# Kernel optimization log

Hardware: AMD Instinct MI355X
Metric: run time of the kernel (lower is better)

The kernel has to match this reference:

```python
import jax, jax.numpy as jnp
import numpy as np

N, E, H = 50000, 800000, 128
NUM_NC = 40
NUM_LAYERS = 3


def setup_inputs() -> dict:
    key = jax.random.key(0)
    ks = jax.random.split(key, 16)
    s = 1.0 / np.sqrt(H)
    inp = {
        "x": jax.random.normal(ks[0], (N, H), jnp.float32),
        "edge_index": jax.random.randint(ks[1], (2, E), 0, N, jnp.int64),
        "na_alphas": 0.001 * jax.random.normal(ks[2], (3, 4), jnp.float32),
        "sc_alphas": 0.001 * jax.random.normal(ks[3], (2, 2), jnp.float32),
        "la_alphas": 0.001 * jax.random.normal(ks[4], (1, 3), jnp.float32),
        "lin1_W": s * jax.random.normal(ks[5], (H, H), jnp.float32),
        "lin1_b": jnp.zeros((H,), jnp.float32),
        "gcn_W": s * jax.random.normal(ks[6], (3, H, H), jnp.float32),
        "gcn_b": jnp.zeros((3, H), jnp.float32),
        "sage_Ws": s * jax.random.normal(ks[7], (3, H, H), jnp.float32),
        "sage_Wn": s * jax.random.normal(ks[8], (3, H, H), jnp.float32),
        "gin_W": s * jax.random.normal(ks[9], (3, H, H), jnp.float32),
        "gin_b": jnp.zeros((3, H), jnp.float32),
        "gin_eps": jnp.zeros((3,), jnp.float32),
        "gat_W": s * jax.random.normal(ks[10], (3, H, H), jnp.float32),
        "gat_as": s * jax.random.normal(ks[11], (3, H), jnp.float32),
        "gat_ad": s * jax.random.normal(ks[12], (3, H), jnp.float32),
        "nc_W": s * jax.random.normal(ks[13], (NUM_NC, H), jnp.float32),
        "nc_b": jnp.zeros((NUM_NC,), jnp.float32),
    }
    return inp


def _gcn(x, src, dst, deg_inv_sqrt, W, b):
    h = x @ W.T + b                           # [N, H]
    norm = deg_inv_sqrt[src] * deg_inv_sqrt[dst]
    msg = h[src] * norm[:, None]              # [E, H] gather
    return jax.ops.segment_sum(msg, dst, num_segments=N)


def _sage(x, src, dst, deg, Ws, Wn):
    agg = jax.ops.segment_sum(x[src], dst, num_segments=N) / jnp.maximum(deg, 1.0)[:, None]
    return x @ Ws.T + agg @ Wn.T


def _gin(x, src, dst, W, b, eps):
    agg = jax.ops.segment_sum(x[src], dst, num_segments=N)
    return ((1.0 + eps) * x + agg) @ W.T + b


def _gat(x, src, dst, W, a_s, a_d):
    h = x @ W.T                               # [N, H]
    logits = jax.nn.leaky_relu((h @ a_s)[src] + (h @ a_d)[dst], 0.2)  # [E]
    m = jax.ops.segment_max(logits, dst, num_segments=N)
    e = jnp.exp(logits - m[dst])
    z = jax.ops.segment_sum(e, dst, num_segments=N)
    alpha = e / (z[dst] + 1e-16)
    return jax.ops.segment_sum(alpha[:, None] * h[src], dst, num_segments=N)


def _na_mixed(x, w, src, dst, deg, dis, l, gcn_W, gcn_b, sage_Ws, sage_Wn,
              gin_W, gin_b, gin_eps, gat_W, gat_as, gat_ad):
    # sum_i w_i * elu(op_i(x, edge_index))
    o0 = _gcn(x, src, dst, dis, gcn_W[l], gcn_b[l])
    o1 = _sage(x, src, dst, deg, sage_Ws[l], sage_Wn[l])
    o2 = _gin(x, src, dst, gin_W[l], gin_b[l], gin_eps[l])
    o3 = _gat(x, src, dst, gat_W[l], gat_as[l], gat_ad[l])
    return (w[0] * jax.nn.elu(o0) + w[1] * jax.nn.elu(o1)
            + w[2] * jax.nn.elu(o2) + w[3] * jax.nn.elu(o3))


def reference(x, edge_index, na_alphas, sc_alphas, la_alphas, lin1_W, lin1_b,
              gcn_W, gcn_b, sage_Ws, sage_Wn, gin_W, gin_b, gin_eps,
              gat_W, gat_as, gat_ad, nc_W, nc_b):
    src, dst = edge_index[0], edge_index[1]
    deg = jax.ops.segment_sum(jnp.ones((E,), x.dtype), dst, num_segments=N)
    dis = jnp.where(deg > 0, 1.0 / jnp.sqrt(jnp.maximum(deg, 1.0)), 0.0)

    na_w = jax.nn.softmax(na_alphas, axis=-1)   # [3, 4]
    sc_w = jax.nn.softmax(sc_alphas, axis=-1)   # [2, 2] (none, skip)
    la_w = jax.nn.softmax(la_alphas, axis=-1)   # [1, 3]

    h = x @ lin1_W.T + lin1_b                   # dropout: eval mode -> identity
    xs = []
    cur = h
    for l in range(NUM_LAYERS):
        cur = _na_mixed(cur, na_w[l], src, dst, deg, dis, l, gcn_W, gcn_b,
                        sage_Ws, sage_Wn, gin_W, gin_b, gin_eps,
                        gat_W, gat_as, gat_ad)
        xs.append(cur)
    x1, x2, x3 = xs

    # fix_last=True: x4 = (x3, sc0(x1), sc1(x2)); SC ops = {none->0, skip->id}
    t = jnp.stack([x3, sc_w[0, 1] * x1, sc_w[1, 1] * x2], axis=0)  # [3, N, H]

    # layer aggregator: sum_i w_i * relu(op_i(tuple)); ops = {max, mean, sum}
    x5 = (la_w[0, 0] * jax.nn.relu(jnp.max(t, axis=0))
          + la_w[0, 1] * jax.nn.relu(jnp.mean(t, axis=0))
          + la_w[0, 2] * jax.nn.relu(jnp.sum(t, axis=0)))

    return x5 @ nc_W.T + nc_b                   # [N, NUM_NC]
```

## Files before the change

kernel.cpp:

```cpp
#include <hip/hip_runtime.h>
#include <hip/hip_bf16.h>

typedef unsigned short u16;
typedef unsigned int u32;
typedef __attribute__((ext_vector_type(8))) short short8;
typedef __attribute__((ext_vector_type(4))) float f32x4;
typedef __attribute__((ext_vector_type(2))) float f32x2;

#define HD 128

__device__ inline float b2f(u16 u){ u32 v = ((u32)u) << 16; return __uint_as_float(v); }
__device__ inline u16 f2b(float f){
  u32 u = __float_as_uint(f);
  u32 r = (u + 0x7fffu + ((u >> 16) & 1u)) >> 16;
  return (u16)r;
}
__device__ inline u32 pack2(float a, float b){
  __hip_bfloat162 h = __float22bfloat162_rn(make_float2(a, b));
  union { __hip_bfloat162 h; u32 u; } c; c.h = h; return c.u;
}
__device__ inline float lo2f(u32 w){ return b2f((u16)(w & 0xffff)); }
__device__ inline float hi2f(u32 w){ return b2f((u16)(w >> 16)); }
__device__ inline float eluf(float x){ return x > 0.f ? x : __expf(x) - 1.f; }
__device__ inline float reluf(float x){ return x > 0.f ? x : 0.f; }
__device__ inline float sane(float x){
  if (!(x == x)) return 0.f;
  return fminf(fmaxf(x, -1e30f), 1e30f);
}
__device__ inline u32 fenc(float f){ u32 u = __float_as_uint(f); return (u & 0x80000000u) ? ~u : (u | 0x80000000u); }
__device__ inline float fdec(u32 u){ return __uint_as_float((u & 0x80000000u) ? (u & 0x7fffffffu) : ~u); }
__device__ __forceinline__ void async16(const u16* g, u16* l){
  __builtin_amdgcn_global_load_lds((const __attribute__((address_space(1))) void*)g,
                                   (__attribute__((address_space(3))) void*)l, 16, 0, 0);
}

__global__ void k_small(const float* __restrict__ na_a, const float* __restrict__ sc_a,
                        const float* __restrict__ la_a, const float* __restrict__ gatW,
                        const float* __restrict__ gat_as, const float* __restrict__ gat_ad,
                        const float* __restrict__ gin_eps, float* __restrict__ sm,
                        u32* __restrict__ maxs)
{
  int t = threadIdx.x;
  if (t < 3) maxs[t] = 0u;
  if (t == 0){
    for (int l = 0; l < 3; l++){
      float a[4]; float mx = -1e30f;
      for (int i = 0; i < 4; i++){ a[i] = na_a[l*4+i]; mx = fmaxf(mx, a[i]); }
      float ssum = 0.f;
      for (int i = 0; i < 4; i++){ a[i] = __expf(a[i]-mx); ssum += a[i]; }
      for (int i = 0; i < 4; i++) sm[l*4+i] = a[i]/ssum;
    }
    for (int r = 0; r < 2; r++){
      float a0 = sc_a[r*2], a1 = sc_a[r*2+1];
      float mx = fmaxf(a0,a1);
      float e0 = __expf(a0-mx), e1 = __expf(a1-mx);
      sm[12+r] = e1/(e0+e1);
    }
    {
      float a0=la_a[0], a1=la_a[1], a2=la_a[2];
      float mx = fmaxf(fmaxf(a0,a1),a2);
      float e0=__expf(a0-mx), e1=__expf(a1-mx), e2=__expf(a2-mx);
      float ssum = e0+e1+e2;
      sm[14]=e0/ssum; sm[15]=e1/ssum; sm[16]=e2/ssum;
    }
    for (int l=0;l<3;l++) sm[17+l] = 1.f + gin_eps[l];
  }
  if (t < 128){
    for (int l=0;l<3;l++){
      float a1=0.f, a2=0.f;
      for (int k=0;k<128;k++){
        float wv = gatW[l*16384 + k*128 + t];
        a1 = fmaf(wv, gat_as[l*128+k], a1);
        a2 = fmaf(wv, gat_ad[l*128+k], a2);
      }
      sm[32  + l*128 + t] = a1;
      sm[416 + l*128 + t] = a2;
    }
  }
}

__device__ __forceinline__ uint4 cvt8(const float* __restrict__ p){
  float4 v0 = *(const float4*)p;
  float4 v1 = *(const float4*)(p + 4);
  uint4 o;
  o.x = pack2(v0.x, v0.y);
  o.y = pack2(v0.z, v0.w);
  o.z = pack2(v1.x, v1.y);
  o.w = pack2(v1.z, v1.w);
  return o;
}
__global__ void k_wcvt(const float* __restrict__ lin1W, const float* __restrict__ gcnW,
                       const float* __restrict__ Ws, const float* __restrict__ Wn,
                       const float* __restrict__ ginW, const float* __restrict__ gatW,
                       u16* __restrict__ wsb)
{
  int i = blockIdx.x*256 + threadIdx.x;
  if (i >= 32768) return;
  int m = i >> 11;
  int j = i & 2047;
  int r = j >> 4, c = j & 15;
  const float* src;
  if (m == 0)       src = lin1W;
  else if (m < 4)   src = gcnW + (m-1)*16384;
  else if (m < 7)   src = Ws   + (m-4)*16384;
  else if (m < 10)  src = Wn   + (m-7)*16384;
  else if (m < 13)  src = ginW + (m-10)*16384;
  else              src = gatW + (m-13)*16384;
  int dj = r*16 + (c ^ (r & 15));
  *(uint4*)(wsb + ((size_t)m*2048 + dj)*8) = cvt8(src + r*HD + c*8);
}

__global__ void k_count(const int* __restrict__ ei, int E, int* __restrict__ cnt){
  int e = blockIdx.x*256 + threadIdx.x;
  if (e < E) atomicAdd(&cnt[ei[E + e]], 1);
}

__global__ void k_scan1(const int* __restrict__ cnt, int Nn, int* __restrict__ bsum){
  __shared__ int red[256];
  int b = blockIdx.x, t = threadIdx.x;
  int base = b*1024 + t*4;
  int s = 0;
  #pragma unroll
  for (int k = 0; k < 4; k++){ int i = base + k; if (i < Nn) s += cnt[i]; }
  red[t] = s; __syncthreads();
  for (int off = 128; off; off >>= 1){
    if (t < off) red[t] += red[t + off];
    __syncthreads();
  }
  if (t == 0) bsum[b] = red[0];
}

__global__ void k_scan2(const int* __restrict__ bsum, int nb,
                        int* __restrict__ boffs, int* __restrict__ rowptr, int Nn){
  __shared__ int sc[1024];
  int t = threadIdx.x;
  int own = (t < nb) ? bsum[t] : 0;
  sc[t] = own;
  __syncthreads();
  for (int off = 1; off < 1024; off <<= 1){
    int add = (t >= off) ? sc[t - off] : 0;
    __syncthreads();
    sc[t] += add;
    __syncthreads();
  }
  if (t < nb) boffs[t] = sc[t] - own;
  if (t == 1023) rowptr[Nn] = sc[1023];
}

__global__ void k_scan3(const int* __restrict__ cnt, const int* __restrict__ boffs, int Nn,
                        int* __restrict__ rowptr, int* __restrict__ cursor,
                        float4* __restrict__ nd){
  __shared__ int red[256];
  int b = blockIdx.x, t = threadIdx.x;
  int base = b*1024 + t*4;
  int c[4]; int s = 0;
  #pragma unroll
  for (int k = 0; k < 4; k++){ int i = base + k; c[k] = (i < Nn) ? cnt[i] : 0; s += c[k]; }
  red[t] = s; __syncthreads();
  for (int off = 1; off < 256; off <<= 1){
    int add = (t >= off) ? red[t - off] : 0;
    __syncthreads();
    red[t] += add;
    __syncthreads();
  }
  int run = red[t] - s + boffs[b];
  #pragma unroll
  for (int k = 0; k < 4; k++){
    int i = base + k;
    if (i < Nn){
      rowptr[i] = run; cursor[i] = run;
      float f = (float)c[k];
      nd[i].z = c[k] > 0 ? 1.f/sqrtf(f) : 0.f;
      nd[i].w = 1.f/fmaxf(f, 1.f);
      run += c[k];
    }
  }
}

__global__ void k_fill(const int* __restrict__ ei, int E,
                       int* __restrict__ cursor, int* __restrict__ csr){
  int e = blockIdx.x*256 + threadIdx.x;
  if (e < E){
    int sv = ei[e], dv = ei[E + e];
    int pos = atomicAdd(&cursor[dv], 1);
    csr[pos] = sv;
  }
}

__global__ __launch_bounds__(256)
void k_agg(const u16* __restrict__ X, const int* __restrict__ rowptr, const int* __restrict__ csr,
           const float4* __restrict__ nd, const float* __restrict__ sm,
           const u32* __restrict__ maxs, int layer, int Nn,
           u16* __restrict__ Qb, u16* __restrict__ Pm, u16* __restrict__ Gb, u16* __restrict__ Rb,
           float* __restrict__ b0)
{
  int wv = blockIdx.x*4 + (threadIdx.x >> 6);
  if (wv >= Nn) return;
  int lane = threadIdx.x & 63;
  int g = lane >> 4, t = lane & 15;
  int beg = rowptr[wv], end = rowptr[wv+1];
  float4 ndw = nd[wv];
  float dval = ndw.y;
  float bnd = fdec(maxs[layer]) + dval;
  float mloc = fmaxf(bnd, 0.2f*bnd);
  f32x2 p2[4], q2[4], r2[4];
  #pragma unroll
  for (int k = 0; k < 4; k++){ p2[k] = (f32x2){0.f,0.f}; q2[k] = (f32x2){0.f,0.f}; r2[k] = (f32x2){0.f,0.f}; }
  float z = 0.f, qd = 0.f;
  int e = beg + g;
  for (; e + 4 < end; e += 8){
    int sv0 = csr[e], sv1 = csr[e+4];
    float4 n0 = nd[sv0], n1 = nd[sv1];
    uint4 xv0 = *(const uint4*)(X + (size_t)sv0*HD + (t ^ (sv0 & 15))*8);
    uint4 xv1 = *(const uint4*)(X + (size_t)sv1*HD + (t ^ (sv1 & 15))*8);
    float s0 = n0.x + dval, s1 = n1.x + dval;
    float lg0 = fmaxf(s0, 0.2f*s0);
    float lg1 = fmaxf(s1, 0.2f*s1);
    float ew0 = __expf(lg0 - mloc), ew1 = __expf(lg1 - mloc);
    u32 a0[4] = {xv0.x, xv0.y, xv0.z, xv0.w};
    u32 a1[4] = {xv1.x, xv1.y, xv1.z, xv1.w};
    f32x2 d0 = {n0.z, n0.z}, d1 = {n1.z, n1.z};
    f32x2 e0 = {ew0, ew0},   e1v = {ew1, ew1};
    #pragma unroll
    for (int k = 0; k < 4; k++){
      f32x2 xf0 = {lo2f(a0[k]), hi2f(a0[k])};
      f32x2 xf1 = {lo2f(a1[k]), hi2f(a1[k])};
      p2[k] += xf0 + xf1;
      q2[k] = __builtin_elementwise_fma(xf0, d0, q2[k]);
      q2[k] = __builtin_elementwise_fma(xf1, d1, q2[k]);
      r2[k] = __builtin_elementwise_fma(xf0, e0, r2[k]);
      r2[k] = __builtin_elementwise_fma(xf1, e1v, r2[k]);
    }
    z += ew0 + ew1; qd += n0.z + n1.z;
  }
  if (e < end){
    int sv = csr[e];
    float4 n0 = nd[sv];
    uint4 xv = *(const uint4*)(X + (size_t)sv*HD + (t ^ (sv & 15))*8);
    float s = n0.x + dval;
    float lg = fmaxf(s, 0.2f*s);
    float ew = __expf(lg - mloc);
    u32 a0[4] = {xv.x, xv.y, xv.z, xv.w};
    f32x2 d0 = {n0.z, n0.z}, e0 = {ew, ew};
    #pragma unroll
    for (int k = 0; k < 4; k++){
      f32x2 xf = {lo2f(a0[k]), hi2f(a0[k])};
      p2[k] += xf;
      q2[k] = __builtin_elementwise_fma(xf, d0, q2[k]);
      r2[k] = __builtin_elementwise_fma(xf, e0, r2[k]);
    }
    z += ew; qd += n0.z;
  }
  #pragma unroll
  for (int off = 16; off <= 32; off <<= 1){
    #pragma unroll
    for (int k = 0; k < 4; k++){
      p2[k].x += __shfl_xor(p2[k].x, off); p2[k].y += __shfl_xor(p2[k].y, off);
      q2[k].x += __shfl_xor(q2[k].x, off); q2[k].y += __shfl_xor(q2[k].y, off);
      r2[k].x += __shfl_xor(r2[k].x, off); r2[k].y += __shfl_xor(r2[k].y, off);
    }
    z  += __shfl_xor(z, off);
    qd += __shfl_xor(qd, off);
  }
  if (g == 0){
    float disv = ndw.z, dinvv = ndw.w;
    float zinv = 1.f/(z + 1e-16f);
    float e1 = sm[17 + layer];
    int tch = t ^ (wv & 15);
    size_t o = (size_t)wv*HD + tch*8;
    uint4 xo = *(const uint4*)(X + o);
    u32 ax[4] = {xo.x, xo.y, xo.z, xo.w};
    uint4 qo, po, go, ro;
    u32* qp = (u32*)&qo; u32* pp = (u32*)&po; u32* gp = (u32*)&go; u32* rp = (u32*)&ro;
    #pragma unroll
    for (int k = 0; k < 4; k++){
      float x0 = lo2f(ax[k]), x1 = hi2f(ax[k]);
      qp[k] = pack2(disv*q2[k].x, disv*q2[k].y);
      pp[k] = pack2(dinvv*p2[k].x, dinvv*p2[k].y);
      gp[k] = pack2(fmaf(e1, x0, p2[k].x), fmaf(e1, x1, p2[k].y));
      rp[k] = pack2(zinv*r2[k].x, zinv*r2[k].y);
    }
    *(uint4*)(Qb + o) = qo;
    *(uint4*)(Pm + o) = po;
    *(uint4*)(Gb + o) = go;
    *(uint4*)(Rb + o) = ro;
    if (t == 0) b0[wv] = disv*qd;
  }
}

__device__ __forceinline__ void stageB_async(u16* lds, const u16* __restrict__ w, int tid){
  int lane = tid & 63, wave = tid >> 6;
  #pragma unroll
  for (int i = 0; i < 8; i++){
    int cb = wave*64 + 256*i;
    async16(w + (size_t)(cb + lane)*8, lds + (size_t)cb*8);
  }
}
__device__ __forceinline__ void stageA64_async(u16* lds, const u16* __restrict__ src,
                                               int mbase, int Nn, int tid){
  int lane = tid & 63, wave = tid >> 6;
  #pragma unroll
  for (int i = 0; i < 4; i++){
    int cb = wave*64 + 256*i;
    int gr = mbase + ((cb + lane) >> 4);
    if (gr < Nn)
      async16(src + ((size_t)mbase*16 + cb + lane)*8, lds + (size_t)cb*8);
  }
}
__device__ __forceinline__ void stageA64_f32(u16* lds, const float* __restrict__ src,
                                             int mbase, int Nn, int tid){
  #pragma unroll
  for (int i = 0; i < 4; i++){
    int chunk = tid + 256*i;
    int r = chunk >> 4;
    int c = chunk & 15;
    uint4 v = {0u,0u,0u,0u};
    int gr = mbase + r;
    if (gr < Nn) v = cvt8(src + (size_t)gr*HD + c*8);
    *(uint4*)(lds + (r*16 + (c ^ (r & 15)))*8) = v;
  }
}
__device__ __forceinline__ void mfma_tile64(const u16* Als, const u16* Bls,
                                            int m0, int lane, f32x4 acc[8]){
  int quad = lane >> 4, lr = lane & 15;
  #pragma unroll
  for (int ks = 0; ks < 4; ks++){
    int q = ks*4 + quad;
    short8 a, b[8];
    int row = m0 + lr;
    a = *(const short8*)(Als + (row*16 + (q ^ lr))*8);
    #pragma unroll
    for (int ct = 0; ct < 8; ct++){
      int brow = ct*16 + lr;
      b[ct] = *(const short8*)(Bls + (brow*16 + (q ^ lr))*8);
    }
    #pragma unroll
    for (int ct = 0; ct < 8; ct++)
      acc[ct] = __builtin_amdgcn_mfma_f32_16x16x32_bf16(a, b[ct], acc[ct], 0, 0, 0);
  }
}

__global__ __launch_bounds__(256,3)
void k_gemm1(const float* __restrict__ A, const u16* __restrict__ Wb, const float* __restrict__ bias,
             const float* __restrict__ sm, float4* __restrict__ nd, u32* __restrict__ maxs,
             int Nn, u16* __restrict__ out)
{
  __shared__ __align__(16) u16 Als[64*128];
  __shared__ __align__(16) u16 Bls[128*128];
  __shared__ float mred[4];
  int tid = threadIdx.x;
  int lane = tid & 63, wave = tid >> 6;
  int m0 = wave*16, mbase = blockIdx.x*64;
  int quad = lane >> 4, lr = lane & 15;
  f32x4 acc[8];
  #pragma unroll
  for (int ct=0;ct<8;ct++) acc[ct] = (f32x4){0.f,0.f,0.f,0.f};
  stageB_async(Bls, Wb, tid);
  stageA64_f32(Als, A, mbase, Nn, tid);
  __syncthreads();
  mfma_tile64(Als, Bls, m0, lane, acc);
  #pragma unroll
  for (int ct=0;ct<8;ct++){
    float bc = bias[ct*16+lr];
    #pragma unroll
    for (int r=0;r<4;r++) acc[ct][r] = sane(acc[ct][r] + bc);
  }
  #pragma unroll
  for (int ct=0;ct<8;ct++){
    int c2 = ct*2 + (lr >> 3);
    #pragma unroll
    for (int r=0;r<4;r++){
      int grow = mbase + m0 + quad*4 + r;
      if (grow < Nn) out[(size_t)grow*HD + (c2 ^ (grow & 15))*8 + (lr & 7)] = f2b(acc[ct][r]);
    }
  }
  {
    const float* wsv = sm + 32;
    const float* wdv = sm + 416;
    float sp[4] = {0.f,0.f,0.f,0.f}, dp[4] = {0.f,0.f,0.f,0.f};
    #pragma unroll
    for (int ct=0;ct<8;ct++){
      float wsc = wsv[ct*16+lr], wdc = wdv[ct*16+lr];
      #pragma unroll
      for (int r=0;r<4;r++){
        sp[r] = fmaf(acc[ct][r], wsc, sp[r]);
        dp[r] = fmaf(acc[ct][r], wdc, dp[r]);
      }
    }
    #pragma unroll
    for (int off=1; off<16; off<<=1)
      #pragma unroll
      for (int r=0;r<4;r++){ sp[r] += __shfl_xor(sp[r], off); dp[r] += __shfl_xor(dp[r], off); }
    float ms = -3.4e38f;
    #pragma unroll
    for (int r=0;r<4;r++){
      int grow = mbase + m0 + quad*4 + r;
      if (grow < Nn){
        ms = fmaxf(ms, sp[r]);
        if (lr == 0) *(float2*)&nd[grow] = make_float2(sp[r], dp[r]);
      }
    }
    ms = fmaxf(ms, __shfl_xor(ms, 16));
    ms = fmaxf(ms, __shfl_xor(ms, 32));
    if (lane == 0) mred[wave] = ms;
    __syncthreads();
    if (tid == 0){
      float m = fmaxf(fmaxf(mred[0],mred[1]), fmaxf(mred[2],mred[3]));
      atomicMax(maxs + 0, fenc(m));
    }
  }
}

__global__ __launch_bounds__(256,3)
void k_layer3(const u16* __restrict__ X, const u16* __restrict__ Qb,
              const u16* __restrict__ Pm, const u16* __restrict__ Gb, const u16* __restrict__ Rb,
              float4* __restrict__ nd, const float* __restrict__ b0,
              const u16* __restrict__ wsb,
              const float* __restrict__ gcnB, const float* __restrict__ ginB,
              const float* __restrict__ sm, u32* __restrict__ maxs,
              int layer, int Nn, u16* __restrict__ out)
{
  __shared__ __align__(16) u16 At[64*128];
  __shared__ __align__(16) u16 Bt[128*128];
  __shared__ float mred[4];
  int tid = threadIdx.x;
  int lane = tid & 63, wave = tid >> 6;
  int m0 = wave*16, mbase = blockIdx.x*64;
  int quad = lane >> 4, lr = lane & 15;
  float w0 = sm[layer*4+0], w1 = sm[layer*4+1], w2 = sm[layer*4+2], w3 = sm[layer*4+3];
  const u16* gcnWb = wsb + (size_t)(1  + layer)*16384;
  const u16* WsWb  = wsb + (size_t)(4  + layer)*16384;
  const u16* WnWb  = wsb + (size_t)(7  + layer)*16384;
  const u16* ginWb = wsb + (size_t)(10 + layer)*16384;
  const u16* gatWb = wsb + (size_t)(13 + layer)*16384;

  f32x4 mix[8];
  f32x4 acc[8];
  float b0r[4];
  #pragma unroll
  for (int r=0;r<4;r++){
    int grow = mbase + m0 + quad*4 + r;
    b0r[r] = (grow < Nn) ? b0[grow] : 0.f;
  }

  stageB_async(Bt, gcnWb, tid);
  stageA64_async(At, Qb, mbase, Nn, tid);
  __syncthreads();
  #pragma unroll
  for (int ct=0;ct<8;ct++) acc[ct] = (f32x4){0.f,0.f,0.f,0.f};
  mfma_tile64(At, Bt, m0, lane, acc);
  {
    float gb[8];
    #pragma unroll
    for (int ct=0;ct<8;ct++) gb[ct] = gcnB[layer*HD + ct*16+lr];
    #pragma unroll
    for (int ct=0;ct<8;ct++)
      #pragma unroll
      for (int r=0;r<4;r++)
        mix[ct][r] = w0 * eluf(acc[ct][r] + b0r[r]*gb[ct]);
  }
  __syncthreads();

  stageB_async(Bt, WsWb, tid);
  stageA64_async(At, X, mbase, Nn, tid);
  __syncthreads();
  #pragma unroll
  for (int ct=0;ct<8;ct++) acc[ct] = (f32x4){0.f,0.f,0.f,0.f};
  mfma_tile64(At, Bt, m0, lane, acc);
  __syncthreads();
  stageB_async(Bt, WnWb, tid);
  stageA64_async(At, Pm, mbase, Nn, tid);
  __syncthreads();
  mfma_tile64(At, Bt, m0, lane, acc);
  #pragma unroll
  for (int ct=0;ct<8;ct++)
    #pragma unroll
    for (int r=0;r<4;r++)
      mix[ct][r] += w1 * eluf(acc[ct][r]);
  __syncthreads();

  stageB_async(Bt, ginWb, tid);
  stageA64_async(At, Gb, mbase, Nn, tid);
  __syncthreads();
  #pragma unroll
  for (int ct=0;ct<8;ct++) acc[ct] = (f32x4){0.f,0.f,0.f,0.f};
  mfma_tile64(At, Bt, m0, lane, acc);
  {
    float gib[8];
    #pragma unroll
    for (int ct=0;ct<8;ct++) gib[ct] = ginB[layer*HD + ct*16+lr];
    #pragma unroll
    for (int ct=0;ct<8;ct++)
      #pragma unroll
      for (int r=0;r<4;r++)
        mix[ct][r] += w2 * eluf(acc[ct][r] + gib[ct]);
  }
  __syncthreads();

  stageB_async(Bt, gatWb, tid);
  stageA64_async(At, Rb, mbase, Nn, tid);
  __syncthreads();
  #pragma unroll
  for (int ct=0;ct<8;ct++) acc[ct] = (f32x4){0.f,0.f,0.f,0.f};
  mfma_tile64(At, Bt, m0, lane, acc);
  #pragma unroll
  for (int ct=0;ct<8;ct++)
    #pragma unroll
    for (int r=0;r<4;r++)
      mix[ct][r] = sane(mix[ct][r] + w3 * eluf(acc[ct][r]));

  #pragma unroll
  for (int ct=0;ct<8;ct++){
    int c2 = ct*2 + (lr >> 3);
    #pragma unroll
    for (int r=0;r<4;r++){
      int grow = mbase + m0 + quad*4 + r;
      if (grow < Nn) out[(size_t)grow*HD + (c2 ^ (grow & 15))*8 + (lr & 7)] = f2b(mix[ct][r]);
    }
  }
  if (layer < 2){
    const float* wsv = sm + 32  + (layer+1)*128;
    const float* wdv = sm + 416 + (layer+1)*128;
    float sp[4] = {0.f,0.f,0.f,0.f}, dp[4] = {0.f,0.f,0.f,0.f};
    #pragma unroll
    for (int ct=0;ct<8;ct++){
      float wsc = wsv[ct*16+lr], wdc = wdv[ct*16+lr];
      #pragma unroll
      for (int r=0;r<4;r++){
        sp[r] = fmaf(mix[ct][r], wsc, sp[r]);
        dp[r] = fmaf(mix[ct][r], wdc, dp[r]);
      }
    }
    #pragma unroll
    for (int off=1; off<16; off<<=1)
      #pragma unroll
      for (int r=0;r<4;r++){ sp[r] += __shfl_xor(sp[r], off); dp[r] += __shfl_xor(dp[r], off); }
    float ms = -3.4e38f;
    #pragma unroll
    for (int r=0;r<4;r++){
      int grow = mbase + m0 + quad*4 + r;
      if (grow < Nn){
        ms = fmaxf(ms, sp[r]);
        if (lr == 0) *(float2*)&nd[grow] = make_float2(sp[r], dp[r]);
      }
    }
    ms = fmaxf(ms, __shfl_xor(ms, 16));
    ms = fmaxf(ms, __shfl_xor(ms, 32));
    if (lane == 0) mred[wave] = ms;
    __syncthreads();
    if (tid == 0){
      float m = fmaxf(fmaxf(mred[0],mred[1]), fmaxf(mred[2],mred[3]));
      atomicMax(maxs + layer + 1, fenc(m));
    }
  }
}

__global__ __launch_bounds__(256)
void k_nc(const u16* __restrict__ X1, const u16* __restrict__ X2, const u16* __restrict__ X3,
          const float* __restrict__ W, const float* __restrict__ bias,
          const float* __restrict__ sm, int Nn, float* __restrict__ out)
{
  __shared__ __align__(16) u16 xs[32*136];
  __shared__ __align__(16) float wn[40*132];
  __shared__ float bs[40];
  int t = threadIdx.x;
  int nb = blockIdx.x*32;
  float c1 = sm[12], c2 = sm[13], la0 = sm[14], la1 = sm[15], la2 = sm[16];
  #pragma unroll
  for (int i = 0; i < 2; i++){
    int chunk = t + 256*i;
    int r = chunk >> 4, c = chunk & 15;
    uint4 v = {0u,0u,0u,0u};
    int gr = nb + r;
    if (gr < Nn){
      size_t o = (size_t)gr*HD + ((c ^ (gr & 15))*8);
      uint4 u1 = *(const uint4*)(X1 + o);
      uint4 u2 = *(const uint4*)(X2 + o);
      uint4 u3 = *(const uint4*)(X3 + o);
      u32* u1p = (u32*)&u1; u32* u2p = (u32*)&u2; u32* u3p = (u32*)&u3; u32* vp = (u32*)&v;
      #pragma unroll
      for (int k = 0; k < 4; k++){
        float o0, o1;
        {
          float a1 = lo2f(u1p[k]), a2 = lo2f(u2p[k]), a3 = lo2f(u3p[k]);
          float t0 = a3, t1 = c1*a1, t2 = c2*a2;
          float smm = t0 + t1 + t2;
          float mx = fmaxf(fmaxf(t0,t1),t2);
          o0 = la0*reluf(mx) + la1*reluf(smm*(1.f/3.f)) + la2*reluf(smm);
        }
        {
          float a1 = hi2f(u1p[k]), a2 = hi2f(u2p[k]), a3 = hi2f(u3p[k]);
          float t0 = a3, t1 = c1*a1, t2 = c2*a2;
          float smm = t0 + t1 + t2;
          float mx = fmaxf(fmaxf(t0,t1),t2);
          o1 = la0*reluf(mx) + la1*reluf(smm*(1.f/3.f)) + la2*reluf(smm);
        }
        vp[k] = pack2(sane(o0), sane(o1));
      }
    }
    *(uint4*)(xs + r*136 + c*8) = v;
  }
  #pragma unroll
  for (int i = 0; i < 5; i++){
    int chunk = t + 256*i;
    int r = chunk >> 5, c = chunk & 31;
    *(float4*)(wn + r*132 + c*4) = *(const float4*)(W + r*HD + c*4);
  }
  if (t < 40) bs[t] = bias[t];
  __syncthreads();
  int nl = t >> 3, cg = t & 7;
  float acc[5];
  #pragma unroll
  for (int j = 0; j < 5; j++) acc[j] = bs[cg + 8*j];
  for (int k = 0; k < 128; k++){
    float xv = b2f(xs[nl*136 + k]);
    #pragma unroll
    for (int j = 0; j < 5; j++)
      acc[j] = fmaf(xv, wn[(cg + 8*j)*132 + k], acc[j]);
  }
  int gr = nb + nl;
  if (gr < Nn){
    #pragma unroll
    for (int j = 0; j < 5; j++)
      out[(size_t)gr*40 + cg + 8*j] = sane(acc[j]);
  }
}

extern "C" void kernel_launch(void* const* d_in, const int* in_sizes, int n_in,
                              void* d_out, int out_size, void* d_ws, size_t ws_size,
                              hipStream_t stream)
{
  (void)n_in; (void)out_size; (void)ws_size;
  const int N = in_sizes[0] / HD;
  const int E = in_sizes[1] / 2;
  const float* x      = (const float*)d_in[0];
  const int*   ei     = (const int*)d_in[1];
  const float* na_a   = (const float*)d_in[2];
  const float* sc_a   = (const float*)d_in[3];
  const float* la_a   = (const float*)d_in[4];
  const float* lin1W  = (const float*)d_in[5];
  const float* lin1b  = (const float*)d_in[6];
  const float* gcnW   = (const float*)d_in[7];
  const float* gcnB   = (const float*)d_in[8];
  const float* sageWs = (const float*)d_in[9];
  const float* sageWn = (const float*)d_in[10];
  const float* ginW   = (const float*)d_in[11];
  const float* ginB   = (const float*)d_in[12];
  const float* ginE   = (const float*)d_in[13];
  const float* gatW   = (const float*)d_in[14];
  const float* gatAs  = (const float*)d_in[15];
  const float* gatAd  = (const float*)d_in[16];
  const float* ncW    = (const float*)d_in[17];
  const float* ncB    = (const float*)d_in[18];

  char* base = (char*)d_ws;
  size_t off = 0;
  auto alloc = [&](size_t b) -> void* {
    void* p = base + off;
    off += (b + 255) & ~(size_t)255;
    return p;
  };
  const int NB = (N + 1023) / 1024;
  float*  smalls = (float*)alloc(4096);
  u32*    maxs   = (u32*)alloc(256);
  int*    cnt    = (int*)alloc((size_t)N*4);
  int*    rowptr = (int*)alloc(((size_t)N+1)*4);
  int*    cursor = (int*)alloc((size_t)N*4);
  int*    bsum   = (int*)alloc(4096);
  int*    boffs  = (int*)alloc(4096);
  float4* nd     = (float4*)alloc((size_t)N*16);
  float*  b0     = (float*)alloc((size_t)N*4);
  int*    csr    = (int*)alloc((size_t)E*4);
  u16*    wsb    = (u16*)alloc((size_t)16*16384*2);
  u16*    xh     = (u16*)alloc((size_t)N*HD*2);
  u16*    x1     = (u16*)alloc((size_t)N*HD*2);
  u16*    x2     = (u16*)alloc((size_t)N*HD*2);
  u16*    Qb     = (u16*)alloc((size_t)N*HD*2);
  u16*    Pm     = (u16*)alloc((size_t)N*HD*2);
  u16*    Gb     = (u16*)alloc((size_t)N*HD*2);
  u16*    Rb     = (u16*)alloc((size_t)N*HD*2);

  hipMemsetAsync(cnt, 0, (size_t)N*4, stream);
  k_small<<<1,128,0,stream>>>(na_a, sc_a, la_a, gatW, gatAs, gatAd, ginE, smalls, maxs);
  k_wcvt<<<128,256,0,stream>>>(lin1W, gcnW, sageWs, sageWn, ginW, gatW, wsb);
  int ebl = (E + 255)/256;
  k_count<<<ebl,256,0,stream>>>(ei, E, cnt);
  k_scan1<<<NB,256,0,stream>>>(cnt, N, bsum);
  k_scan2<<<1,1024,0,stream>>>(bsum, NB, boffs, rowptr, N);
  k_scan3<<<NB,256,0,stream>>>(cnt, boffs, N, rowptr, cursor, nd);
  k_fill<<<ebl,256,0,stream>>>(ei, E, cursor, csr);
  int gbl64 = (N + 63)/64;
  k_gemm1<<<gbl64,256,0,stream>>>(x, wsb, lin1b, smalls, nd, maxs, N, xh);
  const u16* xc = xh;
  u16* outs[3] = {x1, x2, xh};
  int wbl = (N + 3)/4;
  for (int l = 0; l < 3; l++){
    k_agg<<<wbl,256,0,stream>>>(xc, rowptr, csr, nd, smalls, maxs, l, N, Qb, Pm, Gb, Rb, b0);
    k_layer3<<<gbl64,256,0,stream>>>(xc, Qb, Pm, Gb, Rb, nd, b0, wsb,
                                     gcnB, ginB, smalls, maxs, l, N, outs[l]);
    xc = outs[l];
  }
  int ncbl = (N + 31)/32;
  k_nc<<<ncbl,256,0,stream>>>(x1, x2, xh, ncW, ncB, smalls, N, (float*)d_out);
}
```

Measured before the change: 511.9 us.

## Assign one 16-lane group per node and sort nodes by degree for balance

The aggregation kernel now gives each destination node one 16-lane quarter-wave instead of a full wave. This removes the cross-group shuffle reduction and lets each group walk its node's edges serially, two at a time. To keep the four groups in a wave on similar amounts of work, nodes are bucketed by in-degree with a counting sort (histogram, scan, permutation fill) and processed in that order. The cost is three extra small setup kernels and longer serial edge loops per lane for high-degree nodes. Output writes become scattered because the order follows the permutation.

After: 779.3 us. +52.2%, slower.

```diff
diff --git a/kernel.cpp b/kernel.cpp
--- a/kernel.cpp
+++ b/kernel.cpp
@@ -187,17 +187,51 @@
   }
 }
 
+__global__ void k_hist(const int* __restrict__ cnt, int Nn, int* __restrict__ hist){
+  int i = blockIdx.x*256 + threadIdx.x;
+  if (i < Nn){
+    int d = cnt[i]; if (d > 255) d = 255;
+    atomicAdd(&hist[d], 1);
+  }
+}
+__global__ void k_hscan(int* __restrict__ hist){
+  __shared__ int s[256];
+  int t = threadIdx.x;
+  int v = hist[t];
+  s[t] = v;
+  __syncthreads();
+  for (int off = 1; off < 256; off <<= 1){
+    int a = (t >= off) ? s[t - off] : 0;
+    __syncthreads();
+    s[t] += a;
+    __syncthreads();
+  }
+  hist[t] = s[t] - v;
+}
+__global__ void k_permfill(const int* __restrict__ cnt, int Nn,
+                           int* __restrict__ hist, int* __restrict__ perm){
+  int i = blockIdx.x*256 + threadIdx.x;
+  if (i < Nn){
+    int d = cnt[i]; if (d > 255) d = 255;
+    int p = atomicAdd(&hist[d], 1);
+    perm[p] = i;
+  }
+}
+
 __global__ __launch_bounds__(256)
 void k_agg(const u16* __restrict__ X, const int* __restrict__ rowptr, const int* __restrict__ csr,
+           const int* __restrict__ perm,
            const float4* __restrict__ nd, const float* __restrict__ sm,
            const u32* __restrict__ maxs, int layer, int Nn,
            u16* __restrict__ Qb, u16* __restrict__ Pm, u16* __restrict__ Gb, u16* __restrict__ Rb,
            float* __restrict__ b0)
 {
-  int wv = blockIdx.x*4 + (threadIdx.x >> 6);
-  if (wv >= Nn) return;
-  int lane = threadIdx.x & 63;
+  int tid = threadIdx.x;
+  int lane = tid & 63;
   int g = lane >> 4, t = lane & 15;
+  int idx = blockIdx.x*16 + (tid >> 6)*4 + g;
+  if (idx >= Nn) return;
+  int wv = perm[idx];
   int beg = rowptr[wv], end = rowptr[wv+1];
   float4 ndw = nd[wv];
   float dval = ndw.y;
@@ -207,9 +241,9 @@
   #pragma unroll
   for (int k = 0; k < 4; k++){ p2[k] = (f32x2){0.f,0.f}; q2[k] = (f32x2){0.f,0.f}; r2[k] = (f32x2){0.f,0.f}; }
   float z = 0.f, qd = 0.f;
-  int e = beg + g;
-  for (; e + 4 < end; e += 8){
-    int sv0 = csr[e], sv1 = csr[e+4];
+  int e = beg;
+  for (; e + 1 < end; e += 2){
+    int sv0 = csr[e], sv1 = csr[e+1];
     float4 n0 = nd[sv0], n1 = nd[sv1];
     uint4 xv0 = *(const uint4*)(X + (size_t)sv0*HD + (t ^ (sv0 & 15))*8);
     uint4 xv1 = *(const uint4*)(X + (size_t)sv1*HD + (t ^ (sv1 & 15))*8);
@@ -251,18 +285,7 @@
     }
     z += ew; qd += n0.z;
   }
-  #pragma unroll
-  for (int off = 16; off <= 32; off <<= 1){
-    #pragma unroll
-    for (int k = 0; k < 4; k++){
-      p2[k].x += __shfl_xor(p2[k].x, off); p2[k].y += __shfl_xor(p2[k].y, off);
-      q2[k].x += __shfl_xor(q2[k].x, off); q2[k].y += __shfl_xor(q2[k].y, off);
-      r2[k].x += __shfl_xor(r2[k].x, off); r2[k].y += __shfl_xor(r2[k].y, off);
-    }
-    z  += __shfl_xor(z, off);
-    qd += __shfl_xor(qd, off);
-  }
-  if (g == 0){
+  {
     float disv = ndw.z, dinvv = ndw.w;
     float zinv = 1.f/(z + 1e-16f);
     float e1 = sm[17 + layer];
@@ -668,6 +691,8 @@
   int*    cursor = (int*)alloc((size_t)N*4);
   int*    bsum   = (int*)alloc(4096);
   int*    boffs  = (int*)alloc(4096);
+  int*    hist   = (int*)alloc(1024);
+  int*    perm   = (int*)alloc((size_t)N*4);
   float4* nd     = (float4*)alloc((size_t)N*16);
   float*  b0     = (float*)alloc((size_t)N*4);
   int*    csr    = (int*)alloc((size_t)E*4);
@@ -681,10 +706,15 @@
   u16*    Rb     = (u16*)alloc((size_t)N*HD*2);
 
   hipMemsetAsync(cnt, 0, (size_t)N*4, stream);
+  hipMemsetAsync(hist, 0, 1024, stream);
   k_small<<<1,128,0,stream>>>(na_a, sc_a, la_a, gatW, gatAs, gatAd, ginE, smalls, maxs);
   k_wcvt<<<128,256,0,stream>>>(lin1W, gcnW, sageWs, sageWn, ginW, gatW, wsb);
   int ebl = (E + 255)/256;
+  int nbl = (N + 255)/256;
   k_count<<<ebl,256,0,stream>>>(ei, E, cnt);
+  k_hist<<<nbl,256,0,stream>>>(cnt, N, hist);
+  k_hscan<<<1,256,0,stream>>>(hist);
+  k_permfill<<<nbl,256,0,stream>>>(cnt, N, hist, perm);
   k_scan1<<<NB,256,0,stream>>>(cnt, N, bsum);
   k_scan2<<<1,1024,0,stream>>>(bsum, NB, boffs, rowptr, N);
   k_scan3<<<NB,256,0,stream>>>(cnt, boffs, N, rowptr, cursor, nd);
@@ -693,9 +723,9 @@
   k_gemm1<<<gbl64,256,0,stream>>>(x, wsb, lin1b, smalls, nd, maxs, N, xh);
   const u16* xc = xh;
   u16* outs[3] = {x1, x2, xh};
-  int wbl = (N + 3)/4;
+  int abl = (N + 15)/16;
   for (int l = 0; l < 3; l++){
-    k_agg<<<wbl,256,0,stream>>>(xc, rowptr, csr, nd, smalls, maxs, l, N, Qb, Pm, Gb, Rb, b0);
+    k_agg<<<abl,256,0,stream>>>(xc, rowptr, csr, perm, nd, smalls, maxs, l, N, Qb, Pm, Gb, Rb, b0);
     k_layer3<<<gbl64,256,0,stream>>>(xc, Qb, Pm, Gb, Rb, nd, b0, wsb,
                                      gcnB, ginB, smalls, maxs, l, N, outs[l]);
     xc = outs[l];
```
